# Kernel optimization log

Measured on AMD Instinct MI355X. Metric: run time of the kernel, lower is better.

Reference implementation:

```python
import jax, jax.numpy as jnp
import numpy as np

N, E, G = 128000, 2048000, 512
IN, ED, H, C = 12, 2, 64, 10
BN_EPS = 1e-5


def setup_inputs() -> dict:
    key = jax.random.key(0)
    ks = jax.random.split(key, 24)
    p = lambda k, s: (jax.random.normal(k, s, jnp.float32) * 0.05)
    inp = {
        "x": jax.random.normal(ks[0], (N, IN), jnp.float32),
        "edge_index": jax.random.randint(ks[1], (2, E), 0, N),
        "edge_attr": jax.random.normal(ks[2], (E, ED), jnp.float32),
        "batch": jnp.sort(jax.random.randint(ks[3], (N,), 0, G)),
        # edge encoders
        "We1": p(ks[4], (ED, IN)), "be1": jnp.zeros((IN,), jnp.float32),
        "We2": p(ks[5], (ED, H)), "be2": jnp.zeros((H,), jnp.float32),
        "We3": p(ks[6], (ED, H)), "be3": jnp.zeros((H,), jnp.float32),
        # GINE MLPs (Linear + BN eval-mode params)
        "W1": p(ks[7], (IN, H)), "b1": jnp.zeros((H,), jnp.float32),
        "g1": jnp.ones((H,), jnp.float32), "bt1": jnp.zeros((H,), jnp.float32),
        "rm1": jnp.zeros((H,), jnp.float32), "rv1": jnp.ones((H,), jnp.float32),
        "W2": p(ks[8], (H, H)), "b2": jnp.zeros((H,), jnp.float32),
        "g2": jnp.ones((H,), jnp.float32), "bt2": jnp.zeros((H,), jnp.float32),
        "rm2": jnp.zeros((H,), jnp.float32), "rv2": jnp.ones((H,), jnp.float32),
        "W3": p(ks[9], (H, H)), "b3": jnp.zeros((H,), jnp.float32),
        "g3": jnp.ones((H,), jnp.float32), "bt3": jnp.zeros((H,), jnp.float32),
        "rm3": jnp.zeros((H,), jnp.float32), "rv3": jnp.ones((H,), jnp.float32),
        # residual projection
        "Wr": p(ks[10], (IN, H)), "br": jnp.zeros((H,), jnp.float32),
        # classifier
        "Wc1": p(ks[11], (2 * H, H)), "bc1": jnp.zeros((H,), jnp.float32),
        "Wc2": p(ks[12], (H, C)), "bc2": jnp.zeros((C,), jnp.float32),
    }
    return inp


def _bn(h, g, b, rm, rv):
    return g * (h - rm) * jax.lax.rsqrt(rv + BN_EPS) + b


def _gine(x, src, dst, e_emb, W, b, g, bt, rm, rv):
    # message = ReLU(x_j + edge_emb), scatter-sum at target; eps = 0
    msg = jax.nn.relu(x[src] + e_emb)                       # [E, d]
    agg = jax.ops.segment_sum(msg, dst, num_segments=x.shape[0])
    return jax.nn.relu(_bn((x + agg) @ W + b, g, bt, rm, rv))


def reference(x, edge_index, edge_attr, batch,
              We1, be1, We2, be2, We3, be3,
              W1, b1, g1, bt1, rm1, rv1,
              W2, b2, g2, bt2, rm2, rv2,
              W3, b3, g3, bt3, rm3, rv3,
              Wr, br, Wc1, bc1, Wc2, bc2):
    src, dst = edge_index[0], edge_index[1]
    # eval mode: dropout is identity, BN uses running stats
    h = _gine(x, src, dst, edge_attr @ We1 + be1, W1, b1, g1, bt1, rm1, rv1) + (x @ Wr + br)
    h = _gine(h, src, dst, edge_attr @ We2 + be2, W2, b2, g2, bt2, rm2, rv2) + h
    h = _gine(h, src, dst, edge_attr @ We3 + be3, W3, b3, g3, bt3, rm3, rv3) + h
    counts = jax.ops.segment_sum(jnp.ones((h.shape[0],), h.dtype), batch, num_segments=G)
    mean = jax.ops.segment_sum(h, batch, num_segments=G) / jnp.maximum(counts, 1.0)[:, None]
    mx = jax.ops.segment_max(h, batch, num_segments=G)
    mx = jnp.where(counts[:, None] > 0, mx, 0.0)
    pooled = jnp.concatenate([mean, mx], axis=1)            # [G, 2H]
    return jax.nn.relu(pooled @ Wc1 + bc1) @ Wc2 + bc2      # [G, C]
```

## Files before the change

kernel.cpp:

```cpp
#include <hip/hip_runtime.h>
#include <hip/hip_bf16.h>
#include <hip/hip_fp16.h>

#define N_NODES 128000
#define E_EDGES 2048000
#define G_GRAPHS 512
#define D_IN 12
#define D_H 64
#define N_CLS 10
#define BN_EPS 1e-5f
#define NB 1000
#define BCAP 2560
#define TILE 8192
#define NPW 8
#define NPW12 4

typedef _Float16 h2vec __attribute__((ext_vector_type(2)));
typedef _Float16 h4vec __attribute__((ext_vector_type(4)));

__device__ __forceinline__ float fp8_to_f32(int b) {
    return __builtin_amdgcn_cvt_f32_fp8(b, 0);
}
__device__ __forceinline__ unsigned char f32_to_fp8(float v) {
    return (unsigned char)(__builtin_amdgcn_cvt_pk_fp8_f32(v, v, 0, false) & 0xff);
}


__global__ __launch_bounds__(256) void k_bin(const int* __restrict__ src, const int* __restrict__ dst,
                                             const float2* __restrict__ attr, int* __restrict__ gcount,
                                             int2* __restrict__ stage) {
    __shared__ int hist[NB];
    __shared__ int base_s[NB];
    __shared__ int rk[TILE];
    const int t = threadIdx.x;
    const int e0 = blockIdx.x * TILE;
    for (int i = t; i < NB; i += 256) hist[i] = 0;
    __syncthreads();
    for (int i = t; i < TILE; i += 256) {
        int d = dst[e0 + i];
        int b = d >> 7;
        int r = atomicAdd(&hist[b], 1);
        rk[i] = (b << 20) | ((d & 127) << 13) | r;
    }
    __syncthreads();
    for (int i = t; i < NB; i += 256) {
        int cb = hist[i];
        base_s[i] = i * BCAP + ((cb > 0) ? atomicAdd(&gcount[i], cb) : 0);
    }
    __syncthreads();
    for (int i = t; i < TILE; i += 256) {
        int pr = rk[i];
        int b = pr >> 20, dl = (pr >> 13) & 127, r = pr & 8191;
        float2 a = attr[e0 + i];
        __half2 h2 = __floats2half2_rn(a.x, a.y);
        stage[base_s[b] + r] = make_int2(src[e0 + i] | (dl << 17), *(int*)&h2);
    }
}

__global__ __launch_bounds__(256) void k_bscan(const int* __restrict__ gcount, int* __restrict__ bbase,
                                               int* __restrict__ offsets) {
    __shared__ int sm[256];
    const int t = threadIdx.x;
    int c0 = gcount[t * 4], c1 = gcount[t * 4 + 1], c2 = gcount[t * 4 + 2], c3 = gcount[t * 4 + 3];
    int s = c0 + c1 + c2 + c3;
    sm[t] = s;
    __syncthreads();
    for (int off = 1; off < 256; off <<= 1) {
        int x = 0;
        if (t >= off) x = sm[t - off];
        __syncthreads();
        sm[t] += x;
        __syncthreads();
    }
    int base = sm[t] - s;
    if (t * 4 < NB)     bbase[t * 4]     = base;
    if (t * 4 + 1 < NB) bbase[t * 4 + 1] = base + c0;
    if (t * 4 + 2 < NB) bbase[t * 4 + 2] = base + c0 + c1;
    if (t * 4 + 3 < NB) bbase[t * 4 + 3] = base + c0 + c1 + c2;
    if (t == 255) offsets[N_NODES] = sm[255];
}

__global__ __launch_bounds__(256) void k_final(const int* __restrict__ gcount, const int* __restrict__ bbase,
                                               const int2* __restrict__ stage,
                                               int* __restrict__ offsets, int2* __restrict__ edges) {
    __shared__ int2 recs[BCAP];
    __shared__ int cnt[128];
    __shared__ int incl[128];
    const int b = blockIdx.x, t = threadIdx.x;
    const int count = gcount[b];
    const int base = bbase[b];
    if (t < 128) cnt[t] = 0;
    __syncthreads();
    for (int i = t; i < count; i += 256) {
        int2 r = stage[b * BCAP + i];
        recs[i] = r;
        atomicAdd(&cnt[(r.x >> 17) & 127], 1);
    }
    __syncthreads();
    if (t < 128) incl[t] = cnt[t];
    __syncthreads();
    for (int off = 1; off < 128; off <<= 1) {
        int x = 0;
        if (t >= off && t < 128) x = incl[t - off];
        __syncthreads();
        if (t < 128) incl[t] += x;
        __syncthreads();
    }
    if (t < 128) {
        int ex = incl[t] - cnt[t];
        offsets[b * 128 + t] = base + ex;
        cnt[t] = ex;
    }
    __syncthreads();
    for (int i = t; i < count; i += 256) {
        int2 r = recs[i];
        int dl = (r.x >> 17) & 127;
        int p = atomicAdd(&cnt[dl], 1);
        edges[base + p] = make_int2(r.x & 0x1FFFF, r.y);
    }
}

__global__ __launch_bounds__(256) void k_pack_x(const float* __restrict__ x, __half* __restrict__ x16) {
    int idx = blockIdx.x * 256 + threadIdx.x;
    int n = idx >> 4, ch = idx & 15;
    x16[idx] = __float2half((ch < D_IN) ? x[n * D_IN + ch] : 0.f);
}

__global__ __launch_bounds__(256) void k_gine12(
    const float* __restrict__ x, const __half* __restrict__ x16,
    __half* __restrict__ hout, unsigned char* __restrict__ hout8,
    const int* __restrict__ off, const int2* __restrict__ edges,
    const float* __restrict__ We1, const float* __restrict__ be1,
    const float* __restrict__ W1, const float* __restrict__ b1,
    const float* __restrict__ g1, const float* __restrict__ bt1,
    const float* __restrict__ rm1, const float* __restrict__ rv1,
    const float* __restrict__ Wr, const float* __restrict__ br) {
    __shared__ float W1lds[D_IN * 64];
    __shared__ float Wrlds[D_IN * 64];
    __shared__ float u_lds[4][D_IN];
    __shared__ float x_lds[4][D_IN];
    const int t = threadIdx.x, w = t >> 6, c = t & 63;
    const int c15 = c & 15;
    for (int i = t; i < D_IN * 64; i += 256) {
        W1lds[i] = W1[i];
        Wrlds[i] = Wr[i];
    }
    h2vec we2 = {(_Float16)0.f, (_Float16)0.f};
    float bec = 0.f;
    if (c < D_IN) { we2[0] = (_Float16)We1[c]; we2[1] = (_Float16)We1[D_IN + c]; bec = be1[c]; }
    const float sj = g1[c] * rsqrtf(rv1[c] + BN_EPS);
    const float cj = (b1[c] - rm1[c]) * sj + bt1[c];
    const float brj = br[c];
    __syncthreads();

    const int wbase = (blockIdx.x * 4 + w) * NPW12;
    for (int nn = 0; nn < NPW12; ++nn) {
        const int n = wbase + nn;
        const int rs = off[n], re = off[n + 1];
        float acc = 0.f;
        for (int base = rs; base < re; base += 64) {
            const int cnt = min(64, re - base);
            int2 rec = make_int2(0, 0);
            if (c < cnt) rec = edges[base + c];
            for (int j = 0; j < cnt; j += 16) {
                __half hv[16];
                int pkv[16];
#pragma unroll
                for (int u = 0; u < 16; ++u) {
                    int s = __builtin_amdgcn_readlane(rec.x, j + u);
                    pkv[u] = __builtin_amdgcn_readlane(rec.y, j + u);
                    hv[u] = x16[(size_t)s * 16 + c15];
                }
#pragma unroll
                for (int u = 0; u < 16; ++u) {
                    if (j + u < cnt) {
                        float q = __builtin_amdgcn_fdot2(__builtin_bit_cast(h2vec, pkv[u]), we2, bec, false);
                        acc += fmaxf(__half2float(hv[u]) + q, 0.f);
                    }
                }
            }
        }
        if (c < D_IN) {
            float xc = x[(size_t)n * D_IN + c];
            x_lds[w][c] = xc;
            u_lds[w][c] = xc + acc;
        }
        float z = 0.f, r = 0.f;
#pragma unroll
        for (int k = 0; k < D_IN; ++k) {
            z = fmaf(u_lds[w][k], W1lds[k * 64 + c], z);
            r = fmaf(x_lds[w][k], Wrlds[k * 64 + c], r);
        }
        float v = fmaxf(fmaf(z, sj, cj), 0.f) + r + brj;
        hout[(size_t)n * 64 + c] = __float2half(v);
        hout8[(size_t)n * 64 + c] = f32_to_fp8(v);
    }
}

__global__ __launch_bounds__(256) void k_gine64(
    const __half* __restrict__ hin, const unsigned char* __restrict__ hin8,
    __half* __restrict__ hout, unsigned char* __restrict__ hout8,
    const int* __restrict__ off, const int2* __restrict__ edges,
    const float* __restrict__ We, const float* __restrict__ be,
    const float* __restrict__ W, const float* __restrict__ b,
    const float* __restrict__ g, const float* __restrict__ bt,
    const float* __restrict__ rm, const float* __restrict__ rv) {
    __shared__ _Float16 WtL[64][68];
    __shared__ _Float16 uL[4][64];
    const int t = threadIdx.x, w = t >> 6, c = t & 63;
    for (int i = t; i < 4096; i += 256) {
        int k = i >> 6, cc = i & 63;
        WtL[cc][k] = (_Float16)W[i];
    }
    const _Float16 we0h = (_Float16)We[c], we1h = (_Float16)We[64 + c];
    const h2vec we2f = {we0h, we1h};
    const float becf = be[c];
    const float sj = g[c] * rsqrtf(rv[c] + BN_EPS);
    const float cj = (b[c] - rm[c]) * sj + bt[c];
    __syncthreads();

    const int wbase = (blockIdx.x * 4 + w) * NPW;
    for (int nn = 0; nn < NPW; ++nn) {
        const int n = wbase + nn;
        const int rs = off[n], re = off[n + 1];
        const __half hc16 = hin[(size_t)n * 64 + c];
        float acc = 0.f;
        for (int base = rs; base < re; base += 64) {
            const int cnt = min(64, re - base);
            int2 rec = make_int2(0, 0);
            if (c < cnt) rec = edges[base + c];
            for (int j = 0; j < cnt; j += 16) {
                int hvr[16];
#pragma unroll
                for (int u = 0; u < 16; ++u) {
                    int s = __builtin_amdgcn_readlane(rec.x, j + u);
                    hvr[u] = hin8[(size_t)s * 64 + c];
                }
#pragma unroll
                for (int u = 0; u < 16; ++u) {
                    if (j + u < cnt) {
                        int pk = __builtin_amdgcn_readlane(rec.y, j + u);
                        float q = __builtin_amdgcn_fdot2(__builtin_bit_cast(h2vec, pk), we2f, becf, false);
                        acc += fmaxf(fp8_to_f32(hvr[u]) + q, 0.f);
                    }
                }
            }
        }
        const float hc = __half2float(hc16);
        uL[w][c] = (_Float16)(hc + acc);
        float z = 0.f;
        const h4vec* u4p = (const h4vec*)uL[w];
        const h4vec* wt4p = (const h4vec*)&WtL[c][0];
#pragma unroll
        for (int k4 = 0; k4 < 16; ++k4) {
            h4vec uu = u4p[k4];
            h4vec ww = wt4p[k4];
            h2vec ul = __builtin_shufflevector(uu, uu, 0, 1);
            h2vec uh = __builtin_shufflevector(uu, uu, 2, 3);
            h2vec wl = __builtin_shufflevector(ww, ww, 0, 1);
            h2vec wh = __builtin_shufflevector(ww, ww, 2, 3);
            z = __builtin_amdgcn_fdot2(ul, wl, z, false);
            z = __builtin_amdgcn_fdot2(uh, wh, z, false);
        }
        float v = fmaxf(fmaf(z, sj, cj), 0.f) + hc;
        hout[(size_t)n * 64 + c] = __float2half(v);
        hout8[(size_t)n * 64 + c] = f32_to_fp8(v);
    }
}

__global__ __launch_bounds__(256) void k_pool(
    const __half* __restrict__ h, const int* __restrict__ batch,
    const float* __restrict__ Wc1, const float* __restrict__ bc1,
    const float* __restrict__ Wc2, const float* __restrict__ bc2,
    float* __restrict__ out) {
    __shared__ float psum[4][64];
    __shared__ float pmax[4][64];
    __shared__ float pool[128];
    __shared__ float hid[64];
    const int t = threadIdx.x, w = t >> 6, c = t & 63;
    const int g = blockIdx.x;
    int lo = 0, hi = N_NODES;
    while (lo < hi) { int mid = (lo + hi) >> 1; if (batch[mid] < g) lo = mid + 1; else hi = mid; }
    int start = lo;
    hi = N_NODES;
    while (lo < hi) { int mid = (lo + hi) >> 1; if (batch[mid] < g + 1) lo = mid + 1; else hi = mid; }
    int end = lo;

    float s = 0.f, m = -3.4e38f;
    for (int i = start + w; i < end; i += 4) {
        float v = __half2float(h[(size_t)i * 64 + c]);
        s += v;
        m = fmaxf(m, v);
    }
    psum[w][c] = s;
    pmax[w][c] = m;
    __syncthreads();
    if (w == 0) {
        float ss = psum[0][c] + psum[1][c] + psum[2][c] + psum[3][c];
        float mm = fmaxf(fmaxf(pmax[0][c], pmax[1][c]), fmaxf(pmax[2][c], pmax[3][c]));
        int cnt = end - start;
        pool[c] = ss / fmaxf((float)cnt, 1.f);
        pool[64 + c] = (cnt > 0) ? mm : 0.f;
    }
    __syncthreads();
    if (t < 64) {
        float z = bc1[t];
#pragma unroll 8
        for (int k = 0; k < 128; ++k) z = fmaf(pool[k], Wc1[k * 64 + t], z);
        hid[t] = fmaxf(z, 0.f);
    }
    __syncthreads();
    if (t < N_CLS) {
        float z = bc2[t];
#pragma unroll
        for (int k = 0; k < 64; ++k) z = fmaf(hid[k], Wc2[k * N_CLS + t], z);
        out[g * N_CLS + t] = z;
    }
}

extern "C" void kernel_launch(void* const* d_in, const int* in_sizes, int n_in,
                              void* d_out, int out_size, void* d_ws, size_t ws_size,
                              hipStream_t stream) {
    const float* x     = (const float*)d_in[0];
    const int*   ei    = (const int*)d_in[1];
    const float* ea    = (const float*)d_in[2];
    const int*   batch = (const int*)d_in[3];
    const float* We1 = (const float*)d_in[4],  *be1 = (const float*)d_in[5];
    const float* We2 = (const float*)d_in[6],  *be2 = (const float*)d_in[7];
    const float* We3 = (const float*)d_in[8],  *be3 = (const float*)d_in[9];
    const float* W1 = (const float*)d_in[10], *b1 = (const float*)d_in[11];
    const float* g1 = (const float*)d_in[12], *bt1 = (const float*)d_in[13];
    const float* rm1 = (const float*)d_in[14], *rv1 = (const float*)d_in[15];
    const float* W2 = (const float*)d_in[16], *b2 = (const float*)d_in[17];
    const float* g2 = (const float*)d_in[18], *bt2 = (const float*)d_in[19];
    const float* rm2 = (const float*)d_in[20], *rv2 = (const float*)d_in[21];
    const float* W3 = (const float*)d_in[22], *b3 = (const float*)d_in[23];
    const float* g3 = (const float*)d_in[24], *bt3 = (const float*)d_in[25];
    const float* rm3 = (const float*)d_in[26], *rv3 = (const float*)d_in[27];
    const float* Wr = (const float*)d_in[28], *br = (const float*)d_in[29];
    const float* Wc1 = (const float*)d_in[30], *bc1 = (const float*)d_in[31];
    const float* Wc2 = (const float*)d_in[32], *bc2 = (const float*)d_in[33];

    int* off    = (int*)d_ws;
    int* gcount = off + (N_NODES + 4);
    int* bbase  = gcount + 1024;
    int2* edges = (int2*)(bbase + 1024);
    int2* stage = edges + E_EDGES;
    __half* hA  = (__half*)(stage + (size_t)NB * BCAP);
    __half* hB  = hA + (size_t)N_NODES * 64;
    unsigned char* hA8 = (unsigned char*)(hB + (size_t)N_NODES * 64);
    unsigned char* hB8 = hA8 + (size_t)N_NODES * 64;
    __half* x16 = (__half*)(hB8 + (size_t)N_NODES * 64);

    hipMemsetAsync(gcount, 0, 1024 * sizeof(int), stream);

    const int* src = ei;
    const int* dst = ei + E_EDGES;

    k_pack_x<<<N_NODES * 16 / 256, 256, 0, stream>>>(x, x16);
    k_bin<<<E_EDGES / TILE, 256, 0, stream>>>(src, dst, (const float2*)ea, gcount, stage);
    k_bscan<<<1, 256, 0, stream>>>(gcount, bbase, off);
    k_final<<<NB, 256, 0, stream>>>(gcount, bbase, stage, off, edges);

    k_gine12<<<N_NODES / (4 * NPW12), 256, 0, stream>>>(x, x16, hA, hA8, off, edges,
                                                        We1, be1, W1, b1, g1, bt1, rm1, rv1, Wr, br);
    const int g64_blocks = N_NODES / (4 * NPW);
    k_gine64<<<g64_blocks, 256, 0, stream>>>(hA, hA8, hB, hB8, off, edges,
                                             We2, be2, W2, b2, g2, bt2, rm2, rv2);
    k_gine64<<<g64_blocks, 256, 0, stream>>>(hB, hB8, hA, hA8, off, edges,
                                             We3, be3, W3, b3, g3, bt3, rm3, rv3);
    k_pool<<<G_GRAPHS, 256, 0, stream>>>(hA, batch, Wc1, bc1, Wc2, bc2, (float*)d_out);
}
```

Baseline: 490.2 us.

## Gather fp8 neighbor rows as dwords and redistribute via ds_bpermute

In the 64-wide GINE aggregation, each lane now loads a 4-byte word covering four fp8 channels, so one wave fetches 16 neighbor rows per load instruction instead of one row per load. Lanes get their source indices through ds_bpermute, and the loaded words are shuffled back to per-channel lanes with four bpermutes per group, then shifted to pick out the right byte. This replaces 16 byte-wide gather loads per 16 edges with 4 dword loads plus 20 bpermutes. The aim is fewer memory instructions in the gather, paid for with more LDS-crossbar traffic and lane-shuffle work.

```diff
diff --git a/kernel.cpp b/kernel.cpp
--- a/kernel.cpp
+++ b/kernel.cpp
@@ -197,6 +197,31 @@
     }
 }
 
+__device__ __forceinline__ void consume4(int ld, int eb, int cnt, int ry,
+                                         int ad0, int ad1, int ad2, int ad3,
+                                         int shl, h2vec we2f, float becf, float& acc) {
+    int d0 = __builtin_amdgcn_ds_bpermute(ad0, ld);
+    int d1 = __builtin_amdgcn_ds_bpermute(ad1, ld);
+    int d2 = __builtin_amdgcn_ds_bpermute(ad2, ld);
+    int d3 = __builtin_amdgcn_ds_bpermute(ad3, ld);
+    int pk0 = __builtin_amdgcn_readlane(ry, eb + 0);
+    int pk1 = __builtin_amdgcn_readlane(ry, eb + 1);
+    int pk2 = __builtin_amdgcn_readlane(ry, eb + 2);
+    int pk3 = __builtin_amdgcn_readlane(ry, eb + 3);
+    float q0 = __builtin_amdgcn_fdot2(__builtin_bit_cast(h2vec, pk0), we2f, becf, false);
+    float q1 = __builtin_amdgcn_fdot2(__builtin_bit_cast(h2vec, pk1), we2f, becf, false);
+    float q2 = __builtin_amdgcn_fdot2(__builtin_bit_cast(h2vec, pk2), we2f, becf, false);
+    float q3 = __builtin_amdgcn_fdot2(__builtin_bit_cast(h2vec, pk3), we2f, becf, false);
+    float m0 = fmaxf(fp8_to_f32(d0 >> shl) + q0, 0.f);
+    float m1 = fmaxf(fp8_to_f32(d1 >> shl) + q1, 0.f);
+    float m2 = fmaxf(fp8_to_f32(d2 >> shl) + q2, 0.f);
+    float m3 = fmaxf(fp8_to_f32(d3 >> shl) + q3, 0.f);
+    acc += (eb + 0 < cnt) ? m0 : 0.f;
+    acc += (eb + 1 < cnt) ? m1 : 0.f;
+    acc += (eb + 2 < cnt) ? m2 : 0.f;
+    acc += (eb + 3 < cnt) ? m3 : 0.f;
+}
+
 __global__ __launch_bounds__(256) void k_gine64(
     const __half* __restrict__ hin, const unsigned char* __restrict__ hin8,
     __half* __restrict__ hout, unsigned char* __restrict__ hout8,
@@ -217,6 +242,13 @@
     const float becf = be[c];
     const float sj = g[c] * rsqrtf(rv[c] + BN_EPS);
     const float cj = (b[c] - rm[c]) * sj + bt[c];
+    const int asb   = (c >> 4) << 2;
+    const int voffl = (c & 15) << 2;
+    const int ad0   = (c >> 2) << 2;
+    const int ad1   = ad0 + 64;
+    const int ad2   = ad0 + 128;
+    const int ad3   = ad0 + 192;
+    const int shl   = (c & 3) << 3;
     __syncthreads();
 
     const int wbase = (blockIdx.x * 4 + w) * NPW;
@@ -229,21 +261,20 @@
             const int cnt = min(64, re - base);
             int2 rec = make_int2(0, 0);
             if (c < cnt) rec = edges[base + c];
-            for (int j = 0; j < cnt; j += 16) {
-                int hvr[16];
-#pragma unroll
-                for (int u = 0; u < 16; ++u) {
-                    int s = __builtin_amdgcn_readlane(rec.x, j + u);
-                    hvr[u] = hin8[(size_t)s * 64 + c];
-                }
-#pragma unroll
-                for (int u = 0; u < 16; ++u) {
-                    if (j + u < cnt) {
-                        int pk = __builtin_amdgcn_readlane(rec.y, j + u);
-                        float q = __builtin_amdgcn_fdot2(__builtin_bit_cast(h2vec, pk), we2f, becf, false);
-                        acc += fmaxf(fp8_to_f32(hvr[u]) + q, 0.f);
-                    }
-                }
+            for (int j0 = 0; j0 < cnt; j0 += 16) {
+                const int ab = (j0 << 2) + asb;
+                int s0 = __builtin_amdgcn_ds_bpermute(ab,      rec.x);
+                int s1 = __builtin_amdgcn_ds_bpermute(ab + 16, rec.x);
+                int s2 = __builtin_amdgcn_ds_bpermute(ab + 32, rec.x);
+                int s3 = __builtin_amdgcn_ds_bpermute(ab + 48, rec.x);
+                int ld0 = *(const int*)(hin8 + ((s0 << 6) + voffl));
+                int ld1 = *(const int*)(hin8 + ((s1 << 6) + voffl));
+                int ld2 = *(const int*)(hin8 + ((s2 << 6) + voffl));
+                int ld3 = *(const int*)(hin8 + ((s3 << 6) + voffl));
+                consume4(ld0, j0,      cnt, rec.y, ad0, ad1, ad2, ad3, shl, we2f, becf, acc);
+                consume4(ld1, j0 + 4,  cnt, rec.y, ad0, ad1, ad2, ad3, shl, we2f, becf, acc);
+                consume4(ld2, j0 + 8,  cnt, rec.y, ad0, ad1, ad2, ad3, shl, we2f, becf, acc);
+                consume4(ld3, j0 + 12, cnt, rec.y, ad0, ad1, ad2, ad3, shl, we2f, becf, acc);
             }
         }
         const float hc = __half2float(hc16);
```

Measured after the change: 479.1 us. 1.02x faster.

## Gather neighbor rows as dwords across lane groups with sentinel padding node

Applied to the files above, without the earlier changes.

The gather loops in the GINE kernels change from one byte or half per lane per edge to each lane loading a 4-byte dword covering several channels for one of several edges at once. Edge indices are distributed to lanes with ds_bpermute, and per-channel partial sums are reduced with xor shuffles. A sentinel node row (fp8 0xFE / half -30000) is added so padded lanes contribute zero after ReLU, which removes the per-edge bounds check. This cuts the number of gather load instructions and the readlane overhead, at the cost of extra shuffles, LDS round-trips and a dependence on the sentinel value always being clamped by ReLU.

```diff
diff --git a/kernel.cpp b/kernel.cpp
--- a/kernel.cpp
+++ b/kernel.cpp
@@ -18,9 +18,6 @@
 typedef _Float16 h2vec __attribute__((ext_vector_type(2)));
 typedef _Float16 h4vec __attribute__((ext_vector_type(4)));
 
-__device__ __forceinline__ float fp8_to_f32(int b) {
-    return __builtin_amdgcn_cvt_f32_fp8(b, 0);
-}
 __device__ __forceinline__ unsigned char f32_to_fp8(float v) {
     return (unsigned char)(__builtin_amdgcn_cvt_pk_fp8_f32(v, v, 0, false) & 0xff);
 }
@@ -122,8 +119,10 @@
 
 __global__ __launch_bounds__(256) void k_pack_x(const float* __restrict__ x, __half* __restrict__ x16) {
     int idx = blockIdx.x * 256 + threadIdx.x;
+    if (idx >= (N_NODES + 1) * 16) return;
     int n = idx >> 4, ch = idx & 15;
-    x16[idx] = __float2half((ch < D_IN) ? x[n * D_IN + ch] : 0.f);
+    float v = (n == N_NODES) ? -30000.f : ((ch < D_IN) ? x[n * D_IN + ch] : 0.f);
+    x16[idx] = __float2half(v);
 }
 
 __global__ __launch_bounds__(256) void k_gine12(
@@ -137,17 +136,21 @@
     const float* __restrict__ Wr, const float* __restrict__ br) {
     __shared__ float W1lds[D_IN * 64];
     __shared__ float Wrlds[D_IN * 64];
+    __shared__ float uacc[4][16];
     __shared__ float u_lds[4][D_IN];
     __shared__ float x_lds[4][D_IN];
     const int t = threadIdx.x, w = t >> 6, c = t & 63;
-    const int c15 = c & 15;
+    const int asb = (c >> 3) << 2;
+    const int dwoff = (c & 7) << 2;
+    const int ch0 = (c & 7) << 1;
     for (int i = t; i < D_IN * 64; i += 256) {
         W1lds[i] = W1[i];
         Wrlds[i] = Wr[i];
     }
-    h2vec we2 = {(_Float16)0.f, (_Float16)0.f};
-    float bec = 0.f;
-    if (c < D_IN) { we2[0] = (_Float16)We1[c]; we2[1] = (_Float16)We1[D_IN + c]; bec = be1[c]; }
+    h2vec wp0 = {(_Float16)0.f, (_Float16)0.f}, wp1 = wp0;
+    float bp0 = 0.f, bp1 = 0.f;
+    if (ch0 < D_IN)     { wp0[0] = (_Float16)We1[ch0];     wp0[1] = (_Float16)We1[D_IN + ch0];     bp0 = be1[ch0]; }
+    if (ch0 + 1 < D_IN) { wp1[0] = (_Float16)We1[ch0 + 1]; wp1[1] = (_Float16)We1[D_IN + ch0 + 1]; bp1 = be1[ch0 + 1]; }
     const float sj = g1[c] * rsqrtf(rv1[c] + BN_EPS);
     const float cj = (b1[c] - rm1[c]) * sj + bt1[c];
     const float brj = br[c];
@@ -157,33 +160,46 @@
     for (int nn = 0; nn < NPW12; ++nn) {
         const int n = wbase + nn;
         const int rs = off[n], re = off[n + 1];
-        float acc = 0.f;
+        float a0 = 0.f, a1 = 0.f;
         for (int base = rs; base < re; base += 64) {
             const int cnt = min(64, re - base);
-            int2 rec = make_int2(0, 0);
+            int2 rec = make_int2(N_NODES, 0);
             if (c < cnt) rec = edges[base + c];
-            for (int j = 0; j < cnt; j += 16) {
-                __half hv[16];
-                int pkv[16];
-#pragma unroll
-                for (int u = 0; u < 16; ++u) {
-                    int s = __builtin_amdgcn_readlane(rec.x, j + u);
-                    pkv[u] = __builtin_amdgcn_readlane(rec.y, j + u);
-                    hv[u] = x16[(size_t)s * 16 + c15];
+            for (int j0 = 0; j0 < cnt; j0 += 16) {
+                const int ab = (j0 << 2) + asb;
+                int s0 = __builtin_amdgcn_ds_bpermute(ab,      rec.x);
+                int s1 = __builtin_amdgcn_ds_bpermute(ab + 32, rec.x);
+                int e0 = __builtin_amdgcn_ds_bpermute(ab,      rec.y);
+                int e1 = __builtin_amdgcn_ds_bpermute(ab + 32, rec.y);
+                int ld0 = *(const int*)((const char*)x16 + ((s0 << 5) + dwoff));
+                int ld1 = *(const int*)((const char*)x16 + ((s1 << 5) + dwoff));
+                {
+                    h2vec hv = __builtin_bit_cast(h2vec, ld0);
+                    h2vec av = __builtin_bit_cast(h2vec, e0);
+                    float q0 = __builtin_amdgcn_fdot2(av, wp0, bp0, false);
+                    float q1 = __builtin_amdgcn_fdot2(av, wp1, bp1, false);
+                    a0 += fmaxf((float)hv[0] + q0, 0.f);
+                    a1 += fmaxf((float)hv[1] + q1, 0.f);
                 }
-#pragma unroll
-                for (int u = 0; u < 16; ++u) {
-                    if (j + u < cnt) {
-                        float q = __builtin_amdgcn_fdot2(__builtin_bit_cast(h2vec, pkv[u]), we2, bec, false);
-                        acc += fmaxf(__half2float(hv[u]) + q, 0.f);
-                    }
+                {
+                    h2vec hv = __builtin_bit_cast(h2vec, ld1);
+                    h2vec av = __builtin_bit_cast(h2vec, e1);
+                    float q0 = __builtin_amdgcn_fdot2(av, wp0, bp0, false);
+                    float q1 = __builtin_amdgcn_fdot2(av, wp1, bp1, false);
+                    a0 += fmaxf((float)hv[0] + q0, 0.f);
+                    a1 += fmaxf((float)hv[1] + q1, 0.f);
                 }
             }
         }
+        a0 += __shfl_xor(a0, 8);  a1 += __shfl_xor(a1, 8);
+        a0 += __shfl_xor(a0, 16); a1 += __shfl_xor(a1, 16);
+        a0 += __shfl_xor(a0, 32); a1 += __shfl_xor(a1, 32);
+        uacc[w][ch0] = a0;
+        uacc[w][ch0 + 1] = a1;
         if (c < D_IN) {
             float xc = x[(size_t)n * D_IN + c];
             x_lds[w][c] = xc;
-            u_lds[w][c] = xc + acc;
+            u_lds[w][c] = xc + uacc[w][c];
         }
         float z = 0.f, r = 0.f;
 #pragma unroll
@@ -212,9 +228,17 @@
         int k = i >> 6, cc = i & 63;
         WtL[cc][k] = (_Float16)W[i];
     }
-    const _Float16 we0h = (_Float16)We[c], we1h = (_Float16)We[64 + c];
-    const h2vec we2f = {we0h, we1h};
-    const float becf = be[c];
+    const int asb   = (c >> 4) << 2;
+    const int dwoff = (c & 15) << 2;
+    const int q4    = (c & 15) << 2;
+    h2vec weq[4];
+    float beq[4];
+#pragma unroll
+    for (int j = 0; j < 4; ++j) {
+        weq[j][0] = (_Float16)We[q4 + j];
+        weq[j][1] = (_Float16)We[64 + q4 + j];
+        beq[j] = be[q4 + j];
+    }
     const float sj = g[c] * rsqrtf(rv[c] + BN_EPS);
     const float cj = (b[c] - rm[c]) * sj + bt[c];
     __syncthreads();
@@ -223,31 +247,53 @@
     for (int nn = 0; nn < NPW; ++nn) {
         const int n = wbase + nn;
         const int rs = off[n], re = off[n + 1];
-        const __half hc16 = hin[(size_t)n * 64 + c];
-        float acc = 0.f;
+        const float hc = __half2float(hin[(size_t)n * 64 + c]);
+        float acc0 = 0.f, acc1 = 0.f, acc2 = 0.f, acc3 = 0.f;
         for (int base = rs; base < re; base += 64) {
             const int cnt = min(64, re - base);
-            int2 rec = make_int2(0, 0);
+            int2 rec = make_int2(N_NODES, 0);
             if (c < cnt) rec = edges[base + c];
-            for (int j = 0; j < cnt; j += 16) {
-                int hvr[16];
-#pragma unroll
-                for (int u = 0; u < 16; ++u) {
-                    int s = __builtin_amdgcn_readlane(rec.x, j + u);
-                    hvr[u] = hin8[(size_t)s * 64 + c];
+            for (int j0 = 0; j0 < cnt; j0 += 16) {
+                const int ab = (j0 << 2) + asb;
+                int s0 = __builtin_amdgcn_ds_bpermute(ab,      rec.x);
+                int s1 = __builtin_amdgcn_ds_bpermute(ab + 16, rec.x);
+                int s2 = __builtin_amdgcn_ds_bpermute(ab + 32, rec.x);
+                int s3 = __builtin_amdgcn_ds_bpermute(ab + 48, rec.x);
+                int e0 = __builtin_amdgcn_ds_bpermute(ab,      rec.y);
+                int e1 = __builtin_amdgcn_ds_bpermute(ab + 16, rec.y);
+                int e2 = __builtin_amdgcn_ds_bpermute(ab + 32, rec.y);
+                int e3 = __builtin_amdgcn_ds_bpermute(ab + 48, rec.y);
+                int ld0 = *(const int*)(hin8 + ((s0 << 6) + dwoff));
+                int ld1 = *(const int*)(hin8 + ((s1 << 6) + dwoff));
+                int ld2 = *(const int*)(hin8 + ((s2 << 6) + dwoff));
+                int ld3 = *(const int*)(hin8 + ((s3 << 6) + dwoff));
+#define CONSUME(LD, EA)                                                              \
+                {                                                                    \
+                    h2vec av = __builtin_bit_cast(h2vec, EA);                        \
+                    float q0 = __builtin_amdgcn_fdot2(av, weq[0], beq[0], false);    \
+                    float q1 = __builtin_amdgcn_fdot2(av, weq[1], beq[1], false);    \
+                    float q2 = __builtin_amdgcn_fdot2(av, weq[2], beq[2], false);    \
+                    float q3 = __builtin_amdgcn_fdot2(av, weq[3], beq[3], false);    \
+                    acc0 += fmaxf(__builtin_amdgcn_cvt_f32_fp8(LD, 0) + q0, 0.f);    \
+                    acc1 += fmaxf(__builtin_amdgcn_cvt_f32_fp8(LD, 1) + q1, 0.f);    \
+                    acc2 += fmaxf(__builtin_amdgcn_cvt_f32_fp8(LD, 2) + q2, 0.f);    \
+                    acc3 += fmaxf(__builtin_amdgcn_cvt_f32_fp8(LD, 3) + q3, 0.f);    \
                 }
-#pragma unroll
-                for (int u = 0; u < 16; ++u) {
-                    if (j + u < cnt) {
-                        int pk = __builtin_amdgcn_readlane(rec.y, j + u);
-                        float q = __builtin_amdgcn_fdot2(__builtin_bit_cast(h2vec, pk), we2f, becf, false);
-                        acc += fmaxf(fp8_to_f32(hvr[u]) + q, 0.f);
-                    }
-                }
+                CONSUME(ld0, e0)
+                CONSUME(ld1, e1)
+                CONSUME(ld2, e2)
+                CONSUME(ld3, e3)
+#undef CONSUME
             }
         }
-        const float hc = __half2float(hc16);
-        uL[w][c] = (_Float16)(hc + acc);
+        acc0 += __shfl_xor(acc0, 16); acc1 += __shfl_xor(acc1, 16);
+        acc2 += __shfl_xor(acc2, 16); acc3 += __shfl_xor(acc3, 16);
+        acc0 += __shfl_xor(acc0, 32); acc1 += __shfl_xor(acc1, 32);
+        acc2 += __shfl_xor(acc2, 32); acc3 += __shfl_xor(acc3, 32);
+        h4vec aq = {(_Float16)acc0, (_Float16)acc1, (_Float16)acc2, (_Float16)acc3};
+        *(h4vec*)&uL[w][q4] = aq;
+        float u = hc + (float)uL[w][c];
+        uL[w][c] = (_Float16)u;
         float z = 0.f;
         const h4vec* u4p = (const h4vec*)uL[w];
         const h4vec* wt4p = (const h4vec*)&WtL[c][0];
@@ -349,15 +395,17 @@
     __half* hA  = (__half*)(stage + (size_t)NB * BCAP);
     __half* hB  = hA + (size_t)N_NODES * 64;
     unsigned char* hA8 = (unsigned char*)(hB + (size_t)N_NODES * 64);
-    unsigned char* hB8 = hA8 + (size_t)N_NODES * 64;
-    __half* x16 = (__half*)(hB8 + (size_t)N_NODES * 64);
+    unsigned char* hB8 = hA8 + (size_t)(N_NODES + 1) * 64;
+    __half* x16 = (__half*)(hB8 + (size_t)(N_NODES + 1) * 64);
 
     hipMemsetAsync(gcount, 0, 1024 * sizeof(int), stream);
+    hipMemsetAsync(hA8 + (size_t)N_NODES * 64, 0xFE, 64, stream);
+    hipMemsetAsync(hB8 + (size_t)N_NODES * 64, 0xFE, 64, stream);
 
     const int* src = ei;
     const int* dst = ei + E_EDGES;
 
-    k_pack_x<<<N_NODES * 16 / 256, 256, 0, stream>>>(x, x16);
+    k_pack_x<<<((N_NODES + 1) * 16 + 255) / 256, 256, 0, stream>>>(x, x16);
     k_bin<<<E_EDGES / TILE, 256, 0, stream>>>(src, dst, (const float2*)ea, gcount, stage);
     k_bscan<<<1, 256, 0, stream>>>(gcount, bbase, off);
     k_final<<<NB, 256, 0, stream>>>(gcount, bbase, stage, off, edges);
```

Result: faster. 446.9 us (-8.8%).
